# Optimization experiments

Hardware: AMD Instinct MI355X
Metric: run time of the kernel (lower is better)

Reference implementation:

```python
import jax, jax.numpy as jnp
import numpy as np

B, L, HID, H, D = 1, 2048, 3072, 24, 128
MLP = 4 * HID
LH, LW = 32, 56      # latent mask grid -> LH*LW image tokens at the END of the sequence
LIP = 16             # IP-adapter image tokens
IP_SCALE = 0.6


def setup_inputs() -> dict:
    key = jax.random.key(0)
    k = jax.random.split(key, 10)
    # Flux rotary pe layout [1,1,L,D//2,2,2]: pe[...,0]=[cos,-sin], pe[...,1]=[sin,cos]
    pos = jnp.arange(L, dtype=jnp.float32)
    freqs = 1.0 / (10000.0 ** (jnp.arange(0, D, 2, dtype=jnp.float32) / D))
    ang = pos[:, None] * freqs[None, :]            # [L, D//2]
    cos, sin = jnp.cos(ang), jnp.sin(ang)
    pe = jnp.stack([jnp.stack([cos, -sin], -1), jnp.stack([sin, cos], -1)], -2)[None, None]
    return {
        "x": jax.random.normal(k[0], (B, L, HID), jnp.float32),
        "vec": jax.random.normal(k[1], (B, HID), jnp.float32),
        "pe": pe,
        "img_mask": jax.random.uniform(k[2], (B, LH, LW), jnp.float32),
        "image_emb": jax.random.normal(k[3], (B, LIP, HID), jnp.float32),
        "mod_w": jax.random.normal(k[4], (3 * HID, HID), jnp.float32) * 0.02,
        "mod_b": jnp.zeros((3 * HID,), jnp.float32),
        "lin1_w": jax.random.normal(k[5], (3 * HID + MLP, HID), jnp.float32) * 0.02,
        "lin1_b": jnp.zeros((3 * HID + MLP,), jnp.float32),
        "q_scale": jnp.ones((D,), jnp.float32),
        "k_scale": jnp.ones((D,), jnp.float32),
        "lin2_w": jax.random.normal(k[6], (HID, HID + MLP), jnp.float32) * 0.02,
        "lin2_b": jnp.zeros((HID,), jnp.float32),
        "ipk_w": jax.random.normal(k[7], (HID, HID), jnp.float32) * 0.02,
        "ipv_w": jax.random.normal(k[8], (HID, HID), jnp.float32) * 0.02,
    }


def _rms(x, scale, eps):
    # RMSNorm over last dim (QKNorm / norm_added_k)
    return x * jax.lax.rsqrt(jnp.mean(x * x, -1, keepdims=True) + eps) * scale


def _apply_rope(x, pe):
    # x: [B,H,L,D]; pe: [1,1,L,D//2,2,2]
    xr = x.reshape(x.shape[:-1] + (D // 2, 1, 2))
    out = pe[..., 0] * xr[..., 0] + pe[..., 1] * xr[..., 1]  # [B,H,L,D//2,2]
    return out.reshape(x.shape)


def _sdpa(q, k, v):
    # q:[B,H,Lq,D] k,v:[B,H,Lk,D] -> [B,Lq,H*D]
    s = jnp.einsum('bhqd,bhkd->bhqk', q, k) / jnp.sqrt(jnp.float32(D))
    o = jnp.einsum('bhqk,bhkd->bhqd', jax.nn.softmax(s, -1), v)
    return o.transpose(0, 2, 1, 3).reshape(q.shape[0], q.shape[2], H * D)


def reference(x, vec, pe, img_mask, image_emb, mod_w, mod_b, lin1_w, lin1_b,
              q_scale, k_scale, lin2_w, lin2_b, ipk_w, ipv_w):
    # modulation: SiLU(vec) -> Linear -> (shift, scale, gate), each [B,1,HID]
    mod = jax.nn.silu(vec) @ mod_w.T + mod_b
    shift, scale, gate = [m[:, None, :] for m in jnp.split(mod, 3, -1)]
    # pre_norm: LayerNorm, no affine, eps 1e-6 (biased variance, matches torch)
    ln = (x - jnp.mean(x, -1, keepdims=True)) * jax.lax.rsqrt(jnp.var(x, -1, keepdims=True) + 1e-6)
    x_mod = (1.0 + scale) * ln + shift
    # fused qkv + mlp projection
    h = x_mod @ lin1_w.T + lin1_b
    qkv, mlp = h[..., :3 * HID], h[..., 3 * HID:]
    q, k, v = qkv.reshape(B, L, 3, H, D).transpose(2, 0, 3, 1, 4)  # each [B,H,L,D]
    q = _rms(q, q_scale, 1e-6)
    k = _rms(k, k_scale, 1e-6)
    # rp_attention: RoPE then SDPA
    attn = _sdpa(_apply_rope(q, pe), _apply_rope(k, pe), v)       # [B,L,HID]
    # IP-adapter cross-attention: pre-rope q attends to projected image_emb
    ip_k = _rms((image_emb @ ipk_w.T).reshape(B, LIP, H, D).transpose(0, 2, 1, 3), 1.0, 1e-5)
    ip_v = (image_emb @ ipv_w.T).reshape(B, LIP, H, D).transpose(0, 2, 1, 3)
    ip_h = IP_SCALE * _sdpa(q, ip_k, ip_v)                        # [B,L,HID]
    # spatial mask applied to last LH*LW tokens, zeros elsewhere
    full_mask = jnp.concatenate(
        [jnp.zeros((B, L - LH * LW), ip_h.dtype), img_mask.reshape(B, LH * LW)], 1)
    attn = attn + ip_h * full_mask[..., None]
    out = jnp.concatenate([attn, jax.nn.gelu(mlp, approximate=True)], -1) @ lin2_w.T + lin2_b
    return x + gate * out
```

## Files before the change

kernel.cpp:

```cpp
#include <hip/hip_runtime.h>

#define HID 3072
#define LSEQ 2048
#define NH 24
#define HD 128
#define N1 21504
#define K2 15360

typedef unsigned short ushort_t;
typedef __attribute__((ext_vector_type(8))) short bf16x8;
typedef __attribute__((ext_vector_type(4))) float f32x4;

__device__ __forceinline__ unsigned short f2bf(float f) {
    union { float f; unsigned int u; } v; v.f = f;
    unsigned int u = v.u;
    u += 0x7fffu + ((u >> 16) & 1u);
    return (unsigned short)(u >> 16);
}
__device__ __forceinline__ float bf2f(unsigned short s) {
    union { unsigned int u; float f; } v; v.u = ((unsigned int)s) << 16;
    return v.f;
}
__device__ __forceinline__ float gelu_tanh(float x) {
    float u = 0.7978845608028654f * (x + 0.044715f * x * x * x);
    float t = 2.0f / (1.0f + __expf(-2.0f * u)) - 1.0f;
    return 0.5f * x * (1.0f + t);
}
__device__ __forceinline__ void gload_lds16(const ushort_t* g, ushort_t* l) {
    __builtin_amdgcn_global_load_lds((const __attribute__((address_space(1))) void*)g,
                                     (__attribute__((address_space(3))) void*)l, 16, 0, 0);
}

__global__ __launch_bounds__(256) void k_cvt2(const float* __restrict__ s1,
    ushort_t* __restrict__ d1, int n1, const float* __restrict__ s2,
    ushort_t* __restrict__ d2, int n2)
{
    int stride = gridDim.x * 256 * 8;
    int base = (blockIdx.x * 256 + threadIdx.x) * 8;
    for (int i = base; i < n1; i += stride) {
        float4 a = *reinterpret_cast<const float4*>(s1 + i);
        float4 b = *reinterpret_cast<const float4*>(s1 + i + 4);
        uint4 pk;
        pk.x = (unsigned)f2bf(a.x) | ((unsigned)f2bf(a.y) << 16);
        pk.y = (unsigned)f2bf(a.z) | ((unsigned)f2bf(a.w) << 16);
        pk.z = (unsigned)f2bf(b.x) | ((unsigned)f2bf(b.y) << 16);
        pk.w = (unsigned)f2bf(b.z) | ((unsigned)f2bf(b.w) << 16);
        *reinterpret_cast<uint4*>(d1 + i) = pk;
    }
    for (int i = base; i < n2; i += stride) {
        float4 a = *reinterpret_cast<const float4*>(s2 + i);
        float4 b = *reinterpret_cast<const float4*>(s2 + i + 4);
        uint4 pk;
        pk.x = (unsigned)f2bf(a.x) | ((unsigned)f2bf(a.y) << 16);
        pk.y = (unsigned)f2bf(a.z) | ((unsigned)f2bf(a.w) << 16);
        pk.z = (unsigned)f2bf(b.x) | ((unsigned)f2bf(b.y) << 16);
        pk.w = (unsigned)f2bf(b.z) | ((unsigned)f2bf(b.w) << 16);
        *reinterpret_cast<uint4*>(d2 + i) = pk;
    }
}

__global__ __launch_bounds__(256) void k_mod(const float* __restrict__ vec,
    const float* __restrict__ mw, const float* __restrict__ mb, float* __restrict__ mod) {
    __shared__ __align__(16) float sv[HID];
    int tid = threadIdx.x;
    for (int i = tid; i < HID; i += 256) {
        float v = vec[i];
        sv[i] = v / (1.0f + __expf(-v));
    }
    __syncthreads();
    int wave = tid >> 6, lane = tid & 63;
    int n = blockIdx.x * 4 + wave;
    const float* w = mw + (size_t)n * HID;
    float acc = 0.0f;
    for (int k = lane * 4; k < HID; k += 256) {
        float4 wv = *reinterpret_cast<const float4*>(w + k);
        float4 s  = *reinterpret_cast<const float4*>(sv + k);
        acc += wv.x * s.x + wv.y * s.y + wv.z * s.z + wv.w * s.w;
    }
    #pragma unroll
    for (int off = 1; off < 64; off <<= 1) acc += __shfl_xor(acc, off);
    if (lane == 0) mod[n] = acc + mb[n];
}

__global__ __launch_bounds__(256) void k_lnmod(const float* __restrict__ x,
    const float* __restrict__ mod, ushort_t* __restrict__ xmod) {
    int row = blockIdx.x, tid = threadIdx.x;
    const float4* xr = reinterpret_cast<const float4*>(x + (size_t)row * HID);
    float4 v[3];
    float s = 0.f, sq = 0.f;
    #pragma unroll
    for (int i = 0; i < 3; ++i) {
        v[i] = xr[tid + i * 256];
        s  += v[i].x + v[i].y + v[i].z + v[i].w;
        sq += v[i].x * v[i].x + v[i].y * v[i].y + v[i].z * v[i].z + v[i].w * v[i].w;
    }
    #pragma unroll
    for (int off = 1; off < 64; off <<= 1) { s += __shfl_xor(s, off); sq += __shfl_xor(sq, off); }
    __shared__ float rs[4], rq[4];
    int wave = tid >> 6, lane = tid & 63;
    if (lane == 0) { rs[wave] = s; rq[wave] = sq; }
    __syncthreads();
    s  = rs[0] + rs[1] + rs[2] + rs[3];
    sq = rq[0] + rq[1] + rq[2] + rq[3];
    float mean = s * (1.0f / HID);
    float var = sq * (1.0f / HID) - mean * mean;
    float rstd = rsqrtf(var + 1e-6f);
    ushort_t* orow = xmod + (size_t)row * HID;
    #pragma unroll
    for (int i = 0; i < 3; ++i) {
        int c = (tid + i * 256) * 4;
        float4 sc = *reinterpret_cast<const float4*>(mod + HID + c);
        float4 sh = *reinterpret_cast<const float4*>(mod + c);
        float o0 = (1.f + sc.x) * ((v[i].x - mean) * rstd) + sh.x;
        float o1 = (1.f + sc.y) * ((v[i].y - mean) * rstd) + sh.y;
        float o2 = (1.f + sc.z) * ((v[i].z - mean) * rstd) + sh.z;
        float o3 = (1.f + sc.w) * ((v[i].w - mean) * rstd) + sh.w;
        *reinterpret_cast<ushort4*>(orow + c) = make_ushort4(f2bf(o0), f2bf(o1), f2bf(o2), f2bf(o3));
    }
}

#define MFMA_CLUSTER(PH, AF)                                                          \
    do {                                                                              \
        __builtin_amdgcn_s_setprio(1);                                                \
        _Pragma("unroll") for (int i_ = 0; i_ < 2; ++i_)                              \
        _Pragma("unroll") for (int nj_ = 0; nj_ < 4; ++nj_)                           \
        _Pragma("unroll") for (int kh_ = 0; kh_ < 2; ++kh_)                           \
            acc[2 * (PH) + i_][nj_] = __builtin_amdgcn_mfma_f32_16x16x32_bf16(        \
                AF[i_][kh_], bfrag[nj_][kh_], acc[2 * (PH) + i_][nj_], 0, 0, 0);      \
        __builtin_amdgcn_s_setprio(0);                                                \
    } while (0)

template<int EPI>
__global__ __launch_bounds__(512) void k_gemm8(
    const ushort_t* __restrict__ A, const ushort_t* __restrict__ W,
    const float* __restrict__ bias, int Ks, int klen,
    ushort_t* __restrict__ out_qkv, ushort_t* __restrict__ out_concat,
    float* __restrict__ part)
{
    extern __shared__ __align__(16) char smem_raw[];
    ushort_t* smem = (ushort_t*)smem_raw;
    int tid = threadIdx.x;
    int wid = tid >> 6, l = tid & 63;
    int wm = wid >> 2, wn = wid & 3;
    int lr = l & 15, lg = l >> 4;

    int NTILE = (EPI == 1) ? 84 : 12;
    int flat = blockIdx.y * NTILE + blockIdx.x;
    int nf = (flat & 7) * NTILE + (flat >> 3);
    int mt = nf & 7, nt = nf >> 3;
    int m0 = mt * 256, n0 = nt * 256;
    int koff = blockIdx.z * klen;
    int NT = klen >> 6;

    int lrow = l >> 3;
    int lc   = (l & 7) ^ lrow;
    int arow_st = wm * 128 + wn * 32 + lrow;
    int bhalf = wn >> 1, ridx = wm * 2 + (wn & 1);
    int brow_st = bhalf * 128 + ridx * 32 + lrow;
    const ushort_t* aSrc = A + (size_t)(m0 + arow_st) * Ks + koff + lc * 8;
    const ushort_t* bSrc = W + (size_t)(n0 + brow_st) * Ks + koff + lc * 8;
    int aDst = (wm * 128 + wn * 32) * 64;
    int bDst = (bhalf * 128 + ridx * 32) * 64;

    auto stageA = [&](int t, int buf, int c) {
        gload_lds16(aSrc + (size_t)c * 8 * Ks + (size_t)t * 64,
                    smem + buf * 16384 + aDst + c * 512);
    };
    auto stageB = [&](int t, int c) {
        gload_lds16(bSrc + (size_t)c * 8 * Ks + (size_t)t * 64,
                    smem + 49152 + (t & 1) * 16384 + bDst + c * 512);
    };
    auto readA = [&](int buf, int row, int ccc) {
        return *reinterpret_cast<const bf16x8*>(smem + buf * 16384 + row * 64 + ((ccc ^ (row & 7)) << 3));
    };
    auto readB = [&](int p, int row, int ccc) {
        return *reinterpret_cast<const bf16x8*>(smem + 49152 + p * 16384 + row * 64 + ((ccc ^ (row & 7)) << 3));
    };

    f32x4 acc[8][4] = {};

    #pragma unroll
    for (int c = 0; c < 4; ++c) stageA(0, 0, c);
    #pragma unroll
    for (int c = 0; c < 4; ++c) stageB(0, c);
    #pragma unroll
    for (int c = 0; c < 4; ++c) stageA(1, 1, c);
    #pragma unroll
    for (int c = 0; c < 4; ++c) stageB(1, c);
    asm volatile("s_waitcnt vmcnt(8)" ::: "memory");
    __builtin_amdgcn_s_barrier();

    int pA = 0;
    int pA2 = 2;
    for (int t = 0; t < NT; ++t) {
        int pB = t & 1;
        bf16x8 bfrag[4][2], af0[2][2], af1[2][2], af2[2][2], af3[2][2];
        #pragma unroll
        for (int nj = 0; nj < 4; ++nj)
            #pragma unroll
            for (int kh = 0; kh < 2; ++kh)
                bfrag[nj][kh] = readB(pB, wn * 64 + nj * 16 + lr, kh * 4 + lg);
        #pragma unroll
        for (int i = 0; i < 2; ++i)
            #pragma unroll
            for (int kh = 0; kh < 2; ++kh)
                af0[i][kh] = readA(pA, wm * 128 + i * 16 + lr, kh * 4 + lg);
        if (t + 2 < NT) {
            stageA(t + 2, pA2, 0); stageA(t + 2, pA2, 1);
            stageA(t + 2, pA2, 2); stageA(t + 2, pA2, 3);
        }
        #pragma unroll
        for (int i = 0; i < 2; ++i)
            #pragma unroll
            for (int kh = 0; kh < 2; ++kh)
                af1[i][kh] = readA(pA, wm * 128 + (2 + i) * 16 + lr, kh * 4 + lg);
        MFMA_CLUSTER(0, af0);
        #pragma unroll
        for (int i = 0; i < 2; ++i)
            #pragma unroll
            for (int kh = 0; kh < 2; ++kh)
                af2[i][kh] = readA(pA, wm * 128 + (4 + i) * 16 + lr, kh * 4 + lg);
        MFMA_CLUSTER(1, af1);
        __builtin_amdgcn_s_barrier();
        if (t + 2 < NT) {
            stageB(t + 2, 0); stageB(t + 2, 1);
            stageB(t + 2, 2); stageB(t + 2, 3);
        }
        #pragma unroll
        for (int i = 0; i < 2; ++i)
            #pragma unroll
            for (int kh = 0; kh < 2; ++kh)
                af3[i][kh] = readA(pA, wm * 128 + (6 + i) * 16 + lr, kh * 4 + lg);
        MFMA_CLUSTER(2, af2);
        MFMA_CLUSTER(3, af3);
        if (t + 2 < NT)      asm volatile("s_waitcnt vmcnt(8)" ::: "memory");
        else if (t + 1 < NT) asm volatile("s_waitcnt vmcnt(0)" ::: "memory");
        __builtin_amdgcn_s_barrier();
        pA  = (pA  + 1 == 3) ? 0 : pA  + 1;
        pA2 = (pA2 + 1 == 3) ? 0 : pA2 + 1;
    }

    #pragma unroll
    for (int nj = 0; nj < 4; ++nj) {
        int col = n0 + wn * 64 + nj * 16 + lr;
        float b = (EPI == 1) ? bias[col] : 0.f;
        #pragma unroll
        for (int mi = 0; mi < 8; ++mi) {
            int rbase = m0 + wm * 128 + mi * 16 + lg * 4;
            #pragma unroll
            for (int r = 0; r < 4; ++r) {
                int mrow = rbase + r;
                float val = acc[mi][nj][r] + b;
                if (EPI == 1) {
                    if (col < 3 * HID) {
                        out_qkv[(size_t)mrow * (3 * HID) + col] = f2bf(val);
                    } else {
                        out_concat[(size_t)mrow * K2 + HID + (col - 3 * HID)] = f2bf(gelu_tanh(val));
                    }
                } else {
                    part[(size_t)blockIdx.z * LSEQ * HID + (size_t)mrow * HID + col] = val;
                }
            }
        }
    }
}

__global__ __launch_bounds__(256) void k_red(const float* __restrict__ part,
    const float* __restrict__ bias, const float* __restrict__ xres,
    const float* __restrict__ mod, float* __restrict__ dout)
{
    size_t base = ((size_t)blockIdx.x * 256 + threadIdx.x) * 4;
    int col = (int)(base % HID);
    float4 s = *reinterpret_cast<const float4*>(part + base);
    #pragma unroll
    for (int z = 1; z < 4; ++z) {
        float4 p = *reinterpret_cast<const float4*>(part + (size_t)z * LSEQ * HID + base);
        s.x += p.x; s.y += p.y; s.z += p.z; s.w += p.w;
    }
    float4 bb = *reinterpret_cast<const float4*>(bias + col);
    float4 gg = *reinterpret_cast<const float4*>(mod + 2 * HID + col);
    float4 xx = *reinterpret_cast<const float4*>(xres + base);
    float4 o;
    o.x = xx.x + gg.x * (s.x + bb.x);
    o.y = xx.y + gg.y * (s.y + bb.y);
    o.z = xx.z + gg.z * (s.z + bb.z);
    o.w = xx.w + gg.w * (s.w + bb.w);
    *reinterpret_cast<float4*>(dout + base) = o;
}

__global__ __launch_bounds__(256) void k_qkv(const ushort_t* __restrict__ qkv,
    const float* __restrict__ pe, const float* __restrict__ q_scale, const float* __restrict__ k_scale,
    ushort_t* __restrict__ q_rope, ushort_t* __restrict__ k_rope,
    ushort_t* __restrict__ q_rms, ushort_t* __restrict__ v_t)
{
    __shared__ ushort_t vtile[64][132];
    int h = blockIdx.y, l0 = blockIdx.x * 64;
    int wave = threadIdx.x >> 6, lane = threadIdx.x & 63;
    int d0 = lane * 2;
    float qs0 = q_scale[d0], qs1 = q_scale[d0 + 1];
    float ks0 = k_scale[d0], ks1 = k_scale[d0 + 1];
    for (int it = 0; it < 16; ++it) {
        int ll = it * 4 + wave;
        int l = l0 + ll;
        const ushort_t* base = qkv + (size_t)l * (3 * HID) + h * HD + d0;
        unsigned qw = *reinterpret_cast<const unsigned*>(base);
        unsigned kw = *reinterpret_cast<const unsigned*>(base + HID);
        unsigned vw = *reinterpret_cast<const unsigned*>(base + 2 * HID);
        float qx = bf2f((ushort_t)(qw & 0xffffu)), qy = bf2f((ushort_t)(qw >> 16));
        float kx = bf2f((ushort_t)(kw & 0xffffu)), ky = bf2f((ushort_t)(kw >> 16));
        float sq = qx * qx + qy * qy;
        float sk = kx * kx + ky * ky;
        #pragma unroll
        for (int off = 1; off < 64; off <<= 1) { sq += __shfl_xor(sq, off); sk += __shfl_xor(sk, off); }
        float rqv = rsqrtf(sq * (1.0f / HD) + 1e-6f);
        float rkv = rsqrtf(sk * (1.0f / HD) + 1e-6f);
        float qnx = qx * rqv * qs0, qny = qy * rqv * qs1;
        float knx = kx * rkv * ks0, kny = ky * rkv * ks1;
        float4 p = *reinterpret_cast<const float4*>(pe + ((size_t)l * 64 + lane) * 4);
        size_t off_hl = ((size_t)h * LSEQ + l) * HD + d0;
        *reinterpret_cast<unsigned*>(q_rms + off_hl) = (unsigned)f2bf(qnx) | ((unsigned)f2bf(qny) << 16);
        float qrx = p.x * qnx + p.y * qny, qry = p.z * qnx + p.w * qny;
        float krx = p.x * knx + p.y * kny, kry = p.z * knx + p.w * kny;
        *reinterpret_cast<unsigned*>(q_rope + off_hl) = (unsigned)f2bf(qrx) | ((unsigned)f2bf(qry) << 16);
        *reinterpret_cast<unsigned*>(k_rope + off_hl) = (unsigned)f2bf(krx) | ((unsigned)f2bf(kry) << 16);
        vtile[ll][d0] = (ushort_t)(vw & 0xffffu);
        vtile[ll][d0 + 1] = (ushort_t)(vw >> 16);
    }
    __syncthreads();
    int d = threadIdx.x >> 1, half = threadIdx.x & 1;
    ushort_t* dst = v_t + ((size_t)h * HD + d) * LSEQ + l0 + half * 32;
    #pragma unroll
    for (int g = 0; g < 4; ++g) {
        unsigned w0, w1, w2, w3;
        int lb = half * 32 + g * 8;
        w0 = (unsigned)vtile[lb + 0][d] | ((unsigned)vtile[lb + 1][d] << 16);
        w1 = (unsigned)vtile[lb + 2][d] | ((unsigned)vtile[lb + 3][d] << 16);
        w2 = (unsigned)vtile[lb + 4][d] | ((unsigned)vtile[lb + 5][d] << 16);
        w3 = (unsigned)vtile[lb + 6][d] | ((unsigned)vtile[lb + 7][d] << 16);
        reinterpret_cast<uint4*>(dst)[g] = make_uint4(w0, w1, w2, w3);
    }
}

__global__ __launch_bounds__(256) void k_ipgemv(const float* __restrict__ emb,
    const float* __restrict__ wk, const float* __restrict__ wv,
    float* __restrict__ ipk, float* __restrict__ ipv)
{
    int task = blockIdx.x * 4 + (threadIdx.x >> 6);
    int lane = threadIdx.x & 63;
    int which = task / HID;
    int n = task % HID;
    const float* w = (which ? wv : wk) + (size_t)n * HID;
    float acc[16];
    #pragma unroll
    for (int t = 0; t < 16; ++t) acc[t] = 0.f;
    for (int k = lane; k < HID; k += 64) {
        float wval = w[k];
        #pragma unroll
        for (int t = 0; t < 16; ++t) acc[t] += emb[t * HID + k] * wval;
    }
    #pragma unroll
    for (int off = 1; off < 64; off <<= 1) {
        #pragma unroll
        for (int t = 0; t < 16; ++t) acc[t] += __shfl_xor(acc[t], off);
    }
    if (lane == 0) {
        int hh = n >> 7, d = n & 127;
        float* dstp = which ? ipv : ipk;
        #pragma unroll
        for (int t = 0; t < 16; ++t) dstp[((size_t)hh * 16 + t) * HD + d] = acc[t];
    }
}

__global__ __launch_bounds__(256) void k_ipkrms(float* __restrict__ ipk) {
    int row = blockIdx.x * 4 + (threadIdx.x >> 6);
    int lane = threadIdx.x & 63;
    float2 v = *reinterpret_cast<const float2*>(ipk + (size_t)row * HD + lane * 2);
    float sq = v.x * v.x + v.y * v.y;
    #pragma unroll
    for (int off = 1; off < 64; off <<= 1) sq += __shfl_xor(sq, off);
    float r = rsqrtf(sq * (1.0f / HD) + 1e-5f);
    float2 o; o.x = v.x * r; o.y = v.y * r;
    *reinterpret_cast<float2*>(ipk + (size_t)row * HD + lane * 2) = o;
}

__global__ __launch_bounds__(256) void k_attn(const ushort_t* __restrict__ q_rope,
    const ushort_t* __restrict__ k_rope, const ushort_t* __restrict__ v_t,
    float* __restrict__ attnbuf)
{
    __shared__ __align__(16) ushort_t Ks[64 * 128];
    __shared__ __align__(16) ushort_t Vs[128 * 64];
    __shared__ __align__(16) ushort_t Ps[4 * 32 * 72];
    const float SC = 0.08838834764831845f;
    int h = blockIdx.y, q0 = blockIdx.x * 128;
    int tid = threadIdx.x, wave = tid >> 6, lane = tid & 63;
    int lr = lane & 15, lg = lane >> 4;
    const ushort_t* Kb = k_rope + (size_t)h * LSEQ * HD;
    const ushort_t* Vb = v_t + (size_t)h * HD * LSEQ;
    bf16x8 qf[2][4];
    #pragma unroll
    for (int i = 0; i < 2; ++i) {
        #pragma unroll
        for (int ks = 0; ks < 4; ++ks) {
            int row = q0 + wave * 32 + i * 16 + lr;
            int d = ks * 32 + lg * 8;
            qf[i][ks] = *reinterpret_cast<const bf16x8*>(q_rope + ((size_t)h * LSEQ + row) * HD + d);
        }
    }
    f32x4 o[2][8] = {};
    float mrun[2][4], lrun[2][4];
    #pragma unroll
    for (int i = 0; i < 2; ++i)
        #pragma unroll
        for (int r = 0; r < 4; ++r) { mrun[i][r] = -1e30f; lrun[i][r] = 0.f; }

    for (int kt = 0; kt < LSEQ; kt += 64) {
        #pragma unroll
        for (int ii = 0; ii < 4; ++ii) {
            int c = tid + ii * 256;
            int krow = c >> 4, kc = c & 15;
            uint4 va = *reinterpret_cast<const uint4*>(Kb + (size_t)(kt + krow) * HD + kc * 8);
            *reinterpret_cast<uint4*>(reinterpret_cast<char*>(Ks) + krow * 256 + ((kc ^ (krow & 15)) << 4)) = va;
            int dr = c >> 3, vc = c & 7;
            uint4 vb = *reinterpret_cast<const uint4*>(Vb + (size_t)dr * LSEQ + kt + vc * 8);
            *reinterpret_cast<uint4*>(reinterpret_cast<char*>(Vs) + dr * 128 + ((vc ^ (dr & 7)) << 4)) = vb;
        }
        __syncthreads();
        f32x4 s[2][4] = {};
        __builtin_amdgcn_s_setprio(1);
        #pragma unroll
        for (int ks = 0; ks < 4; ++ks) {
            bf16x8 kf[4];
            #pragma unroll
            for (int j = 0; j < 4; ++j) {
                int krow = j * 16 + lr;
                int cc = ks * 4 + lg;
                kf[j] = *reinterpret_cast<const bf16x8*>(reinterpret_cast<char*>(Ks) + krow * 256 + ((cc ^ (krow & 15)) << 4));
            }
            #pragma unroll
            for (int i = 0; i < 2; ++i)
                #pragma unroll
                for (int j = 0; j < 4; ++j)
                    s[i][j] = __builtin_amdgcn_mfma_f32_16x16x32_bf16(qf[i][ks], kf[j], s[i][j], 0, 0, 0);
        }
        __builtin_amdgcn_s_setprio(0);
        float alpha[2][4];
        #pragma unroll
        for (int i = 0; i < 2; ++i) {
            #pragma unroll
            for (int r = 0; r < 4; ++r) {
                float v0 = s[i][0][r] * SC, v1 = s[i][1][r] * SC;
                float v2 = s[i][2][r] * SC, v3 = s[i][3][r] * SC;
                float mx = fmaxf(fmaxf(v0, v1), fmaxf(v2, v3));
                #pragma unroll
                for (int off = 1; off < 16; off <<= 1) mx = fmaxf(mx, __shfl_xor(mx, off));
                float mnew = fmaxf(mrun[i][r], mx);
                float al = __expf(mrun[i][r] - mnew);
                float p0 = __expf(v0 - mnew), p1 = __expf(v1 - mnew);
                float p2 = __expf(v2 - mnew), p3 = __expf(v3 - mnew);
                float rs2 = p0 + p1 + p2 + p3;
                #pragma unroll
                for (int off = 1; off < 16; off <<= 1) rs2 += __shfl_xor(rs2, off);
                lrun[i][r] = lrun[i][r] * al + rs2;
                mrun[i][r] = mnew;
                alpha[i][r] = al;
                s[i][0][r] = p0; s[i][1][r] = p1; s[i][2][r] = p2; s[i][3][r] = p3;
            }
        }
        #pragma unroll
        for (int i = 0; i < 2; ++i)
            #pragma unroll
            for (int j8 = 0; j8 < 8; ++j8)
                #pragma unroll
                for (int r = 0; r < 4; ++r) o[i][j8][r] *= alpha[i][r];
        #pragma unroll
        for (int i = 0; i < 2; ++i)
            #pragma unroll
            for (int j = 0; j < 4; ++j)
                #pragma unroll
                for (int r = 0; r < 4; ++r) {
                    int ql = i * 16 + lg * 4 + r;
                    int kp = j * 16 + lr;
                    Ps[wave * 2304 + ql * 72 + kp] = f2bf(s[i][j][r]);
                }
        __syncthreads();
        bf16x8 pa[2][2];
        #pragma unroll
        for (int i = 0; i < 2; ++i)
            #pragma unroll
            for (int ks2 = 0; ks2 < 2; ++ks2)
                pa[i][ks2] = *reinterpret_cast<const bf16x8*>(Ps + wave * 2304 + (i * 16 + lr) * 72 + ks2 * 32 + lg * 8);
        __builtin_amdgcn_s_setprio(1);
        #pragma unroll
        for (int j8 = 0; j8 < 8; ++j8) {
            int d = j8 * 16 + lr;
            #pragma unroll
            for (int ks2 = 0; ks2 < 2; ++ks2) {
                int cc = ks2 * 4 + lg;
                bf16x8 vf = *reinterpret_cast<const bf16x8*>(reinterpret_cast<char*>(Vs) + d * 128 + ((cc ^ (d & 7)) << 4));
                #pragma unroll
                for (int i = 0; i < 2; ++i)
                    o[i][j8] = __builtin_amdgcn_mfma_f32_16x16x32_bf16(pa[i][ks2], vf, o[i][j8], 0, 0, 0);
            }
        }
        __builtin_amdgcn_s_setprio(0);
        __syncthreads();
    }
    #pragma unroll
    for (int i = 0; i < 2; ++i) {
        #pragma unroll
        for (int r = 0; r < 4; ++r) {
            float inv = 1.0f / lrun[i][r];
            int mrow = q0 + wave * 32 + i * 16 + lg * 4 + r;
            float* orow = attnbuf + (size_t)mrow * HID + h * HD;
            #pragma unroll
            for (int j8 = 0; j8 < 8; ++j8)
                orow[j8 * 16 + lr] = o[i][j8][r] * inv;
        }
    }
}

__global__ __launch_bounds__(256) void k_ipattn(const ushort_t* __restrict__ q_rms,
    const float* __restrict__ ipk, const float* __restrict__ ipv,
    const float* __restrict__ attnbuf, const float* __restrict__ img_mask,
    ushort_t* __restrict__ concat)
{
    int task = blockIdx.x * 4 + (threadIdx.x >> 6);
    int lane = threadIdx.x & 63;
    int h = task >> 11;
    int l = task & 2047;
    int d0 = lane * 2;
    float2 a = *reinterpret_cast<const float2*>(attnbuf + (size_t)l * HID + h * HD + d0);
    if (l >= 256) {
        float mask = img_mask[l - 256];
        unsigned qv = *reinterpret_cast<const unsigned*>(q_rms + ((size_t)h * LSEQ + l) * HD + d0);
        float qx = bf2f((unsigned short)(qv & 0xffffu)), qy = bf2f((unsigned short)(qv >> 16));
        float s[16];
        const float* kb = ipk + (size_t)h * 16 * HD + d0;
        #pragma unroll
        for (int j = 0; j < 16; ++j) {
            float2 kk = *reinterpret_cast<const float2*>(kb + j * HD);
            float part = qx * kk.x + qy * kk.y;
            #pragma unroll
            for (int off = 1; off < 64; off <<= 1) part += __shfl_xor(part, off);
            s[j] = part * 0.08838834764831845f;
        }
        float mx = s[0];
        #pragma unroll
        for (int j = 1; j < 16; ++j) mx = fmaxf(mx, s[j]);
        float sum = 0.f;
        #pragma unroll
        for (int j = 0; j < 16; ++j) { s[j] = __expf(s[j] - mx); sum += s[j]; }
        float ox = 0.f, oy = 0.f;
        const float* vb = ipv + (size_t)h * 16 * HD + d0;
        #pragma unroll
        for (int j = 0; j < 16; ++j) {
            float2 vv = *reinterpret_cast<const float2*>(vb + j * HD);
            ox += s[j] * vv.x; oy += s[j] * vv.y;
        }
        float f = 0.6f * mask / sum;
        a.x += f * ox; a.y += f * oy;
    }
    *reinterpret_cast<unsigned*>(concat + (size_t)l * K2 + h * HD + d0) =
        (unsigned)f2bf(a.x) | ((unsigned)f2bf(a.y) << 16);
}

extern "C" void kernel_launch(void* const* d_in, const int* in_sizes, int n_in,
                              void* d_out, int out_size, void* d_ws, size_t ws_size,
                              hipStream_t stream)
{
    (void)in_sizes; (void)n_in; (void)out_size; (void)ws_size;
    const float* x         = (const float*)d_in[0];
    const float* vec       = (const float*)d_in[1];
    const float* pe        = (const float*)d_in[2];
    const float* img_mask  = (const float*)d_in[3];
    const float* image_emb = (const float*)d_in[4];
    const float* mod_w     = (const float*)d_in[5];
    const float* mod_b     = (const float*)d_in[6];
    const float* lin1_w    = (const float*)d_in[7];
    const float* lin1_b    = (const float*)d_in[8];
    const float* q_scale   = (const float*)d_in[9];
    const float* k_scale   = (const float*)d_in[10];
    const float* lin2_w    = (const float*)d_in[11];
    const float* lin2_b    = (const float*)d_in[12];
    const float* ipk_w     = (const float*)d_in[13];
    const float* ipv_w     = (const float*)d_in[14];
    float* dout = (float*)d_out;

    char* wp = (char*)d_ws;
    auto alloc = [&](size_t bytes) { char* p = wp; wp += (bytes + 255) & ~(size_t)255; return p; };
    float*    mod     = (float*)   alloc((size_t)9216 * 4);
    ushort_t* concat  = (ushort_t*)alloc((size_t)LSEQ * K2 * 2);
    ushort_t* lin2_bf = (ushort_t*)alloc((size_t)HID * K2 * 2);
    float*    ipk     = (float*)   alloc((size_t)NH * 16 * HD * 4);
    float*    ipv     = (float*)   alloc((size_t)NH * 16 * HD * 4);
    char* ubase = wp;
    ushort_t* lin1_bf = (ushort_t*)alloc((size_t)N1 * HID * 2);
    ushort_t* xmod    = (ushort_t*)alloc((size_t)LSEQ * HID * 2);
    ushort_t* qkv     = (ushort_t*)alloc((size_t)LSEQ * 3 * HID * 2);
    float*    attnbuf = (float*)   alloc((size_t)LSEQ * HID * 4);
    ushort_t* q_rope  = (ushort_t*)alloc((size_t)NH * LSEQ * HD * 2);
    ushort_t* k_rope  = (ushort_t*)alloc((size_t)NH * LSEQ * HD * 2);
    ushort_t* q_rms   = (ushort_t*)alloc((size_t)NH * LSEQ * HD * 2);
    ushort_t* v_t     = (ushort_t*)alloc((size_t)NH * HD * LSEQ * 2);
    float*    partial = (float*)ubase;

    hipFuncSetAttribute((const void*)k_gemm8<1>, hipFuncAttributeMaxDynamicSharedMemorySize, 163840);
    hipFuncSetAttribute((const void*)k_gemm8<0>, hipFuncAttributeMaxDynamicSharedMemorySize, 163840);

    k_cvt2  <<<dim3(4096), dim3(256), 0, stream>>>(lin1_w, lin1_bf, N1 * HID,
                                                   lin2_w, lin2_bf, HID * K2);
    k_mod   <<<dim3(9216 / 4), dim3(256), 0, stream>>>(vec, mod_w, mod_b, mod);
    k_lnmod <<<dim3(LSEQ), dim3(256), 0, stream>>>(x, mod, xmod);
    k_gemm8<1><<<dim3(84, 8, 1), dim3(512), 163840, stream>>>(xmod, lin1_bf, lin1_b, HID, HID,
                                                              qkv, concat, nullptr);
    k_qkv   <<<dim3(32, NH), dim3(256), 0, stream>>>(qkv, pe, q_scale, k_scale,
                                                     q_rope, k_rope, q_rms, v_t);
    k_ipgemv<<<dim3(2 * HID / 4), dim3(256), 0, stream>>>(image_emb, ipk_w, ipv_w, ipk, ipv);
    k_ipkrms<<<dim3(NH * 16 / 4), dim3(256), 0, stream>>>(ipk);
    k_attn  <<<dim3(16, NH), dim3(256), 0, stream>>>(q_rope, k_rope, v_t, attnbuf);
    k_ipattn<<<dim3(NH * LSEQ / 4), dim3(256), 0, stream>>>(q_rms, ipk, ipv, attnbuf, img_mask, concat);
    k_gemm8<0><<<dim3(12, 8, 4), dim3(512), 163840, stream>>>(concat, lin2_bf, nullptr, K2, 3840,
                                                              nullptr, nullptr, partial);
    k_red   <<<dim3(LSEQ * HID / 1024), dim3(256), 0, stream>>>(partial, lin2_b, x, mod, dout);
}
```

Baseline: 1.069 ms.

## Add 128x128 split-K GEMM for lin2 with bf16 partials; prefetch KV in attention

Replaces the 256x256 split-K lin2 GEMM with a dedicated 128x128-tile, 256-thread kernel that uses smaller shared memory, so more blocks run per CU. Split-K partial sums are stored as bf16 instead of fp32, and the reduction kernel is widened to handle 8 elements per thread. This halves partial-buffer traffic at some cost in accumulation precision. The attention kernel now prefetches the next K/V tile into registers while computing on the current one, and remaps block indices for better cache locality.

After: 1.132 ms. 1.06x slower.

```diff
diff --git a/kernel.cpp b/kernel.cpp
--- a/kernel.cpp
+++ b/kernel.cpp
@@ -130,35 +130,32 @@
         __builtin_amdgcn_s_setprio(0);                                                \
     } while (0)
 
-template<int EPI>
 __global__ __launch_bounds__(512) void k_gemm8(
     const ushort_t* __restrict__ A, const ushort_t* __restrict__ W,
-    const float* __restrict__ bias, int Ks, int klen,
-    ushort_t* __restrict__ out_qkv, ushort_t* __restrict__ out_concat,
-    float* __restrict__ part)
+    const float* __restrict__ bias,
+    ushort_t* __restrict__ out_qkv, ushort_t* __restrict__ out_concat)
 {
     extern __shared__ __align__(16) char smem_raw[];
     ushort_t* smem = (ushort_t*)smem_raw;
+    const int Ks = HID;
     int tid = threadIdx.x;
     int wid = tid >> 6, l = tid & 63;
     int wm = wid >> 2, wn = wid & 3;
     int lr = l & 15, lg = l >> 4;
 
-    int NTILE = (EPI == 1) ? 84 : 12;
-    int flat = blockIdx.y * NTILE + blockIdx.x;
-    int nf = (flat & 7) * NTILE + (flat >> 3);
+    int flat = blockIdx.y * 84 + blockIdx.x;
+    int nf = (flat & 7) * 84 + (flat >> 3);
     int mt = nf & 7, nt = nf >> 3;
     int m0 = mt * 256, n0 = nt * 256;
-    int koff = blockIdx.z * klen;
-    int NT = klen >> 6;
+    int NT = Ks >> 6;
 
     int lrow = l >> 3;
     int lc   = (l & 7) ^ lrow;
     int arow_st = wm * 128 + wn * 32 + lrow;
     int bhalf = wn >> 1, ridx = wm * 2 + (wn & 1);
     int brow_st = bhalf * 128 + ridx * 32 + lrow;
-    const ushort_t* aSrc = A + (size_t)(m0 + arow_st) * Ks + koff + lc * 8;
-    const ushort_t* bSrc = W + (size_t)(n0 + brow_st) * Ks + koff + lc * 8;
+    const ushort_t* aSrc = A + (size_t)(m0 + arow_st) * Ks + lc * 8;
+    const ushort_t* bSrc = W + (size_t)(n0 + brow_st) * Ks + lc * 8;
     int aDst = (wm * 128 + wn * 32) * 64;
     int bDst = (bhalf * 128 + ridx * 32) * 64;
 
@@ -190,8 +187,7 @@
     asm volatile("s_waitcnt vmcnt(8)" ::: "memory");
     __builtin_amdgcn_s_barrier();
 
-    int pA = 0;
-    int pA2 = 2;
+    int pA = 0, pA2 = 2;
     for (int t = 0; t < NT; ++t) {
         int pB = t & 1;
         bf16x8 bfrag[4][2], af0[2][2], af1[2][2], af2[2][2], af3[2][2];
@@ -243,7 +239,7 @@
     #pragma unroll
     for (int nj = 0; nj < 4; ++nj) {
         int col = n0 + wn * 64 + nj * 16 + lr;
-        float b = (EPI == 1) ? bias[col] : 0.f;
+        float b = bias[col];
         #pragma unroll
         for (int mi = 0; mi < 8; ++mi) {
             int rbase = m0 + wm * 128 + mi * 16 + lg * 4;
@@ -251,41 +247,159 @@
             for (int r = 0; r < 4; ++r) {
                 int mrow = rbase + r;
                 float val = acc[mi][nj][r] + b;
-                if (EPI == 1) {
-                    if (col < 3 * HID) {
-                        out_qkv[(size_t)mrow * (3 * HID) + col] = f2bf(val);
-                    } else {
-                        out_concat[(size_t)mrow * K2 + HID + (col - 3 * HID)] = f2bf(gelu_tanh(val));
-                    }
+                if (col < 3 * HID) {
+                    out_qkv[(size_t)mrow * (3 * HID) + col] = f2bf(val);
                 } else {
-                    part[(size_t)blockIdx.z * LSEQ * HID + (size_t)mrow * HID + col] = val;
+                    out_concat[(size_t)mrow * K2 + HID + (col - 3 * HID)] = f2bf(gelu_tanh(val));
                 }
             }
         }
     }
 }
 
-__global__ __launch_bounds__(256) void k_red(const float* __restrict__ part,
+#define MFMA_CL4(PH, AF)                                                              \
+    do {                                                                              \
+        __builtin_amdgcn_s_setprio(1);                                                \
+        _Pragma("unroll") for (int nj_ = 0; nj_ < 4; ++nj_)                           \
+        _Pragma("unroll") for (int kh_ = 0; kh_ < 2; ++kh_)                           \
+            acc[(PH)][nj_] = __builtin_amdgcn_mfma_f32_16x16x32_bf16(                 \
+                AF[kh_], bfrag[nj_][kh_], acc[(PH)][nj_], 0, 0, 0);                   \
+        __builtin_amdgcn_s_setprio(0);                                                \
+    } while (0)
+
+__global__ __launch_bounds__(256) void k_gemm4(
+    const ushort_t* __restrict__ A, const ushort_t* __restrict__ W,
+    int klen, ushort_t* __restrict__ part)
+{
+    extern __shared__ __align__(16) char smem_raw[];
+    ushort_t* smem = (ushort_t*)smem_raw;
+    const int Ks = K2;
+    int tid = threadIdx.x;
+    int wave = tid >> 6, l = tid & 63;
+    int wm = wave >> 1, wn = wave & 1;
+    int lr = l & 15, lg = l >> 4;
+
+    int flat = blockIdx.y * 24 + blockIdx.x;
+    int nf = (flat & 7) * 48 + (flat >> 3);
+    int mt = nf & 15, nt = nf >> 4;
+    int m0 = mt * 128, n0 = nt * 128;
+    int koff = blockIdx.z * klen;
+    int NT = klen >> 6;
+
+    int lrow = l >> 3;
+    int lc   = (l & 7) ^ lrow;
+    const ushort_t* aSrc = A + (size_t)(m0 + wave * 32 + lrow) * Ks + koff + lc * 8;
+    const ushort_t* bSrc = W + (size_t)(n0 + wave * 32 + lrow) * Ks + koff + lc * 8;
+    int dstBase = wave * 2048;
+
+    auto stageA = [&](int t, int buf) {
+        #pragma unroll
+        for (int c = 0; c < 4; ++c)
+            gload_lds16(aSrc + (size_t)c * 8 * Ks + (size_t)t * 64,
+                        smem + buf * 8192 + dstBase + c * 512);
+    };
+    auto stageB = [&](int t) {
+        #pragma unroll
+        for (int c = 0; c < 4; ++c)
+            gload_lds16(bSrc + (size_t)c * 8 * Ks + (size_t)t * 64,
+                        smem + 24576 + (t & 1) * 8192 + dstBase + c * 512);
+    };
+    auto readA = [&](int buf, int row, int ccc) {
+        return *reinterpret_cast<const bf16x8*>(smem + buf * 8192 + row * 64 + ((ccc ^ (row & 7)) << 3));
+    };
+    auto readB = [&](int p, int row, int ccc) {
+        return *reinterpret_cast<const bf16x8*>(smem + 24576 + p * 8192 + row * 64 + ((ccc ^ (row & 7)) << 3));
+    };
+
+    f32x4 acc[4][4] = {};
+
+    stageA(0, 0); stageB(0); stageA(1, 1); stageB(1);
+    asm volatile("s_waitcnt vmcnt(8)" ::: "memory");
+    __builtin_amdgcn_s_barrier();
+
+    int pA = 0, pA2 = 2;
+    for (int t = 0; t < NT; ++t) {
+        int pB = t & 1;
+        bf16x8 bfrag[4][2], af0[2], af1[2], af2[2], af3[2];
+        #pragma unroll
+        for (int nj = 0; nj < 4; ++nj)
+            #pragma unroll
+            for (int kh = 0; kh < 2; ++kh)
+                bfrag[nj][kh] = readB(pB, wn * 64 + nj * 16 + lr, kh * 4 + lg);
+        #pragma unroll
+        for (int kh = 0; kh < 2; ++kh)
+            af0[kh] = readA(pA, wm * 64 + lr, kh * 4 + lg);
+        if (t + 2 < NT) stageA(t + 2, pA2);
+        #pragma unroll
+        for (int kh = 0; kh < 2; ++kh)
+            af1[kh] = readA(pA, wm * 64 + 16 + lr, kh * 4 + lg);
+        MFMA_CL4(0, af0);
+        #pragma unroll
+        for (int kh = 0; kh < 2; ++kh)
+            af2[kh] = readA(pA, wm * 64 + 32 + lr, kh * 4 + lg);
+        MFMA_CL4(1, af1);
+        __builtin_amdgcn_s_barrier();
+        if (t + 2 < NT) stageB(t + 2);
+        #pragma unroll
+        for (int kh = 0; kh < 2; ++kh)
+            af3[kh] = readA(pA, wm * 64 + 48 + lr, kh * 4 + lg);
+        MFMA_CL4(2, af2);
+        MFMA_CL4(3, af3);
+        if (t + 2 < NT)      asm volatile("s_waitcnt vmcnt(8)" ::: "memory");
+        else if (t + 1 < NT) asm volatile("s_waitcnt vmcnt(0)" ::: "memory");
+        __builtin_amdgcn_s_barrier();
+        pA  = (pA  + 1 == 3) ? 0 : pA  + 1;
+        pA2 = (pA2 + 1 == 3) ? 0 : pA2 + 1;
+    }
+
+    #pragma unroll
+    for (int nj = 0; nj < 4; ++nj) {
+        int col = n0 + wn * 64 + nj * 16 + lr;
+        #pragma unroll
+        for (int mi = 0; mi < 4; ++mi) {
+            int rbase = m0 + wm * 64 + mi * 16 + lg * 4;
+            #pragma unroll
+            for (int r = 0; r < 4; ++r) {
+                int mrow = rbase + r;
+                part[(size_t)blockIdx.z * LSEQ * HID + (size_t)mrow * HID + col] = f2bf(acc[mi][nj][r]);
+            }
+        }
+    }
+}
+
+__global__ __launch_bounds__(256) void k_red(const ushort_t* __restrict__ part,
     const float* __restrict__ bias, const float* __restrict__ xres,
     const float* __restrict__ mod, float* __restrict__ dout)
 {
-    size_t base = ((size_t)blockIdx.x * 256 + threadIdx.x) * 4;
+    size_t base = ((size_t)blockIdx.x * 256 + threadIdx.x) * 8;
     int col = (int)(base % HID);
-    float4 s = *reinterpret_cast<const float4*>(part + base);
-    #pragma unroll
-    for (int z = 1; z < 4; ++z) {
-        float4 p = *reinterpret_cast<const float4*>(part + (size_t)z * LSEQ * HID + base);
-        s.x += p.x; s.y += p.y; s.z += p.z; s.w += p.w;
-    }
-    float4 bb = *reinterpret_cast<const float4*>(bias + col);
-    float4 gg = *reinterpret_cast<const float4*>(mod + 2 * HID + col);
-    float4 xx = *reinterpret_cast<const float4*>(xres + base);
-    float4 o;
-    o.x = xx.x + gg.x * (s.x + bb.x);
-    o.y = xx.y + gg.y * (s.y + bb.y);
-    o.z = xx.z + gg.z * (s.z + bb.z);
-    o.w = xx.w + gg.w * (s.w + bb.w);
-    *reinterpret_cast<float4*>(dout + base) = o;
+    float s[8] = {0.f, 0.f, 0.f, 0.f, 0.f, 0.f, 0.f, 0.f};
+    #pragma unroll
+    for (int z = 0; z < 4; ++z) {
+        uint4 pv = *reinterpret_cast<const uint4*>(part + (size_t)z * LSEQ * HID + base);
+        unsigned w0 = pv.x, w1 = pv.y, w2 = pv.z, w3 = pv.w;
+        s[0] += bf2f((ushort_t)(w0 & 0xffffu)); s[1] += bf2f((ushort_t)(w0 >> 16));
+        s[2] += bf2f((ushort_t)(w1 & 0xffffu)); s[3] += bf2f((ushort_t)(w1 >> 16));
+        s[4] += bf2f((ushort_t)(w2 & 0xffffu)); s[5] += bf2f((ushort_t)(w2 >> 16));
+        s[6] += bf2f((ushort_t)(w3 & 0xffffu)); s[7] += bf2f((ushort_t)(w3 >> 16));
+    }
+    float4 bb0 = *reinterpret_cast<const float4*>(bias + col);
+    float4 bb1 = *reinterpret_cast<const float4*>(bias + col + 4);
+    float4 gg0 = *reinterpret_cast<const float4*>(mod + 2 * HID + col);
+    float4 gg1 = *reinterpret_cast<const float4*>(mod + 2 * HID + col + 4);
+    float4 xx0 = *reinterpret_cast<const float4*>(xres + base);
+    float4 xx1 = *reinterpret_cast<const float4*>(xres + base + 4);
+    float4 o0, o1;
+    o0.x = xx0.x + gg0.x * (s[0] + bb0.x);
+    o0.y = xx0.y + gg0.y * (s[1] + bb0.y);
+    o0.z = xx0.z + gg0.z * (s[2] + bb0.z);
+    o0.w = xx0.w + gg0.w * (s[3] + bb0.w);
+    o1.x = xx1.x + gg1.x * (s[4] + bb1.x);
+    o1.y = xx1.y + gg1.y * (s[5] + bb1.y);
+    o1.z = xx1.z + gg1.z * (s[6] + bb1.z);
+    o1.w = xx1.w + gg1.w * (s[7] + bb1.w);
+    *reinterpret_cast<float4*>(dout + base) = o0;
+    *reinterpret_cast<float4*>(dout + base + 4) = o1;
 }
 
 __global__ __launch_bounds__(256) void k_qkv(const ushort_t* __restrict__ qkv,
@@ -391,7 +505,9 @@
     __shared__ __align__(16) ushort_t Vs[128 * 64];
     __shared__ __align__(16) ushort_t Ps[4 * 32 * 72];
     const float SC = 0.08838834764831845f;
-    int h = blockIdx.y, q0 = blockIdx.x * 128;
+    int flat = blockIdx.y * 16 + blockIdx.x;
+    int nf = (flat & 7) * 48 + (flat >> 3);
+    int h = nf >> 4, q0 = (nf & 15) << 7;
     int tid = threadIdx.x, wave = tid >> 6, lane = tid & 63;
     int lr = lane & 15, lg = lane >> 4;
     const ushort_t* Kb = k_rope + (size_t)h * LSEQ * HD;
@@ -413,18 +529,30 @@
         #pragma unroll
         for (int r = 0; r < 4; ++r) { mrun[i][r] = -1e30f; lrun[i][r] = 0.f; }
 
-    for (int kt = 0; kt < LSEQ; kt += 64) {
+    uint4 kreg[4], vreg[4];
+    auto loadKV = [&](int kt) {
         #pragma unroll
         for (int ii = 0; ii < 4; ++ii) {
             int c = tid + ii * 256;
             int krow = c >> 4, kc = c & 15;
-            uint4 va = *reinterpret_cast<const uint4*>(Kb + (size_t)(kt + krow) * HD + kc * 8);
-            *reinterpret_cast<uint4*>(reinterpret_cast<char*>(Ks) + krow * 256 + ((kc ^ (krow & 15)) << 4)) = va;
+            kreg[ii] = *reinterpret_cast<const uint4*>(Kb + (size_t)(kt + krow) * HD + kc * 8);
             int dr = c >> 3, vc = c & 7;
-            uint4 vb = *reinterpret_cast<const uint4*>(Vb + (size_t)dr * LSEQ + kt + vc * 8);
-            *reinterpret_cast<uint4*>(reinterpret_cast<char*>(Vs) + dr * 128 + ((vc ^ (dr & 7)) << 4)) = vb;
+            vreg[ii] = *reinterpret_cast<const uint4*>(Vb + (size_t)dr * LSEQ + kt + vc * 8);
+        }
+    };
+    loadKV(0);
+
+    for (int kt = 0; kt < LSEQ; kt += 64) {
+        #pragma unroll
+        for (int ii = 0; ii < 4; ++ii) {
+            int c = tid + ii * 256;
+            int krow = c >> 4, kc = c & 15;
+            *reinterpret_cast<uint4*>(reinterpret_cast<char*>(Ks) + krow * 256 + ((kc ^ (krow & 15)) << 4)) = kreg[ii];
+            int dr = c >> 3, vc = c & 7;
+            *reinterpret_cast<uint4*>(reinterpret_cast<char*>(Vs) + dr * 128 + ((vc ^ (dr & 7)) << 4)) = vreg[ii];
         }
         __syncthreads();
+        if (kt + 64 < LSEQ) loadKV(kt + 64);
         f32x4 s[2][4] = {};
         __builtin_amdgcn_s_setprio(1);
         #pragma unroll
@@ -602,24 +730,22 @@
     ushort_t* k_rope  = (ushort_t*)alloc((size_t)NH * LSEQ * HD * 2);
     ushort_t* q_rms   = (ushort_t*)alloc((size_t)NH * LSEQ * HD * 2);
     ushort_t* v_t     = (ushort_t*)alloc((size_t)NH * HD * LSEQ * 2);
-    float*    partial = (float*)ubase;
-
-    hipFuncSetAttribute((const void*)k_gemm8<1>, hipFuncAttributeMaxDynamicSharedMemorySize, 163840);
-    hipFuncSetAttribute((const void*)k_gemm8<0>, hipFuncAttributeMaxDynamicSharedMemorySize, 163840);
+    ushort_t* partial = (ushort_t*)ubase;
+
+    hipFuncSetAttribute((const void*)k_gemm8, hipFuncAttributeMaxDynamicSharedMemorySize, 163840);
+    hipFuncSetAttribute((const void*)k_gemm4, hipFuncAttributeMaxDynamicSharedMemorySize, 81920);
 
     k_cvt2  <<<dim3(4096), dim3(256), 0, stream>>>(lin1_w, lin1_bf, N1 * HID,
                                                    lin2_w, lin2_bf, HID * K2);
     k_mod   <<<dim3(9216 / 4), dim3(256), 0, stream>>>(vec, mod_w, mod_b, mod);
     k_lnmod <<<dim3(LSEQ), dim3(256), 0, stream>>>(x, mod, xmod);
-    k_gemm8<1><<<dim3(84, 8, 1), dim3(512), 163840, stream>>>(xmod, lin1_bf, lin1_b, HID, HID,
-                                                              qkv, concat, nullptr);
+    k_gemm8 <<<dim3(84, 8), dim3(512), 163840, stream>>>(xmod, lin1_bf, lin1_b, qkv, concat);
     k_qkv   <<<dim3(32, NH), dim3(256), 0, stream>>>(qkv, pe, q_scale, k_scale,
                                                      q_rope, k_rope, q_rms, v_t);
     k_ipgemv<<<dim3(2 * HID / 4), dim3(256), 0, stream>>>(image_emb, ipk_w, ipv_w, ipk, ipv);
     k_ipkrms<<<dim3(NH * 16 / 4), dim3(256), 0, stream>>>(ipk);
     k_attn  <<<dim3(16, NH), dim3(256), 0, stream>>>(q_rope, k_rope, v_t, attnbuf);
     k_ipattn<<<dim3(NH * LSEQ / 4), dim3(256), 0, stream>>>(q_rms, ipk, ipv, attnbuf, img_mask, concat);
-    k_gemm8<0><<<dim3(12, 8, 4), dim3(512), 163840, stream>>>(concat, lin2_bf, nullptr, K2, 3840,
-                                                              nullptr, nullptr, partial);
-    k_red   <<<dim3(LSEQ * HID / 1024), dim3(256), 0, stream>>>(partial, lin2_b, x, mod, dout);
-}
+    k_gemm4 <<<dim3(24, 16, 4), dim3(256), 81920, stream>>>(concat, lin2_bf, 3840, partial);
+    k_red   <<<dim3(LSEQ * HID / 2048), dim3(256), 0, stream>>>(partial, lin2_b, x, mod, dout);
+}
```
